# Performance work log

Measured on AMD Instinct MI355X. Metric: run time of the kernel, lower is better.

The kernel has to match this reference:

```python
import jax, jax.numpy as jnp
import numpy as np

B, V_IN, V_OUT, C_IN, C_OUT, K, NNZ = 16, 1024, 4096, 128, 256, 18, 16384

def setup_inputs() -> dict:
    key = jax.random.key(0)
    ks = jax.random.split(key, 10)
    def lin(k, fan_in, fan_out):
        s = 1.0 / np.sqrt(fan_in)
        return jax.random.normal(k, (fan_in, fan_out), jnp.float32) * s
    return {
        "x": jax.random.normal(ks[0], (B, V_IN, C_IN), jnp.float32),
        "vals": jax.random.uniform(ks[1], (NNZ,), jnp.float32),
        "W1": lin(ks[2], 1 * C_IN, C_OUT),
        "b1": jnp.zeros((C_OUT,), jnp.float32),
        "Wd3": lin(ks[3], (K // 3) * C_IN, C_OUT // 4),
        "bd3": jnp.zeros((C_OUT // 4,), jnp.float32),
        "W2d3": lin(ks[4], (K // 3 * 2) * C_IN, C_OUT // 4),
        "b2d3": jnp.zeros((C_OUT // 4,), jnp.float32),
        "Wf": lin(ks[5], K * C_IN, C_OUT // 2),
        "bf": jnp.zeros((C_OUT // 2,), jnp.float32),
        "rows": jax.random.randint(ks[6], (NNZ,), 0, V_OUT, jnp.int32),
        "cols": jax.random.randint(ks[7], (NNZ,), 0, V_IN, jnp.int32),
        "spiral_idx": jax.random.randint(ks[8], (V_OUT, K), 0, V_OUT, jnp.int32),
    }

def _pool(x, rows, cols, vals, dim_size):
    # sparse upsample: gather cols, scale, scatter-add to rows
    gathered = x[:, cols, :] * vals[None, :, None]  # [B, nnz, C]
    return jnp.zeros((x.shape[0], dim_size, x.shape[2]), x.dtype).at[:, rows, :].add(gathered)

def _spiral_conv(feat, idx, W, b):
    # gather fixed spiral neighborhoods then shared linear layer
    Bz, V, C = feat.shape[0], idx.shape[0], feat.shape[2]
    g = feat[:, idx.reshape(-1), :].reshape(Bz, V, idx.shape[1] * C)  # [B, V, K*C]
    return g @ W + b

def reference(x, vals, W1, b1, Wd3, bd3, W2d3, b2d3, Wf, bf, rows, cols, spiral_idx):
    out = _pool(x, rows, cols, vals, V_OUT)  # [B, V_OUT, C_IN]
    k = spiral_idx.shape[1]
    short_cut = _spiral_conv(out, spiral_idx[:, :1], W1, b1)
    p_d3 = _spiral_conv(out, spiral_idx[:, : k // 3], Wd3, bd3)
    p_2d3 = _spiral_conv(out, spiral_idx[:, : k // 3 * 2], W2d3, b2d3)
    p = _spiral_conv(out, spiral_idx, Wf, bf)
    f = jnp.concatenate((p, p_2d3, p_d3), axis=2)  # [B, V_OUT, C_OUT]
    return jax.nn.relu(short_cut + f)
```

## Files before the change

kernel.cpp:

```cpp
#include <hip/hip_runtime.h>
#include <hip/hip_bf16.h>

#define B_SZ   16
#define V_IN   1024
#define V_OUT  4096
#define C_IN   128
#define C_OUT  256
#define K_NB   18
#define NNZ    16384
#define K_GEMM (K_NB * C_IN)
#define BK     64
#define NKT    (K_GEMM / BK)

typedef __attribute__((ext_vector_type(8))) short bf16x8;
typedef __attribute__((ext_vector_type(4))) float f32x4;

#define GLOAD16(src, dst) __builtin_amdgcn_global_load_lds( \
    (const __attribute__((address_space(1))) unsigned int*)(src), \
    (__attribute__((address_space(3))) unsigned int*)(dst), 16, 0, 0)

__global__ void hist_kernel(const int* __restrict__ rows, int* counts) {
    int n = blockIdx.x * blockDim.x + threadIdx.x;
    if (n < NNZ) atomicAdd(&counts[rows[n]], 1);
}

__global__ void scan_kernel(const int* __restrict__ counts, int* offsets, int* cursor) {
    __shared__ int wsum[16];
    int t = threadIdx.x;
    int lane = t & 63, wid = t >> 6;
    int base4 = t * 4;
    int c0 = counts[base4], c1 = counts[base4 + 1], c2 = counts[base4 + 2], c3 = counts[base4 + 3];
    int tot = c0 + c1 + c2 + c3;
    int v = tot;
#pragma unroll
    for (int d = 1; d < 64; d <<= 1) {
        int u = __shfl_up(v, d);
        if (lane >= d) v += u;
    }
    if (lane == 63) wsum[wid] = v;
    __syncthreads();
    int wbase = 0;
#pragma unroll
    for (int w = 0; w < 16; ++w) wbase += (w < wid) ? wsum[w] : 0;
    int incl = wbase + v;
    int excl = incl - tot;
    offsets[base4]     = excl;
    offsets[base4 + 1] = excl + c0;
    offsets[base4 + 2] = excl + c0 + c1;
    offsets[base4 + 3] = excl + c0 + c1 + c2;
    cursor[base4]     = excl;
    cursor[base4 + 1] = excl + c0;
    cursor[base4 + 2] = excl + c0 + c1;
    cursor[base4 + 3] = excl + c0 + c1 + c2;
    if (t == 1023) offsets[V_OUT] = incl;
}

__global__ void fill_kernel(const int* __restrict__ rows, int* cursor, int* perm) {
    int n = blockIdx.x * blockDim.x + threadIdx.x;
    if (n < NNZ) {
        int r = rows[n];
        int pos = atomicAdd(&cursor[r], 1);
        perm[pos] = n;
    }
}

__global__ __launch_bounds__(128) void pool_kernel(
    const float* __restrict__ x, const float* __restrict__ vals,
    const int* __restrict__ cols, const int* __restrict__ offsets,
    const int* __restrict__ perm, __hip_bfloat16* __restrict__ pool) {
    int r = blockIdx.x;
    int c = threadIdx.x;
    int j0 = offsets[r], j1 = offsets[r + 1];
    float acc[B_SZ];
#pragma unroll
    for (int b = 0; b < B_SZ; ++b) acc[b] = 0.f;
    for (int j = j0; j < j1; ++j) {
        int n = perm[j];
        float v = vals[n];
        const float* xp = x + (size_t)cols[n] * C_IN + c;
#pragma unroll
        for (int b = 0; b < B_SZ; ++b) acc[b] += v * xp[(size_t)b * V_IN * C_IN];
    }
#pragma unroll
    for (int b = 0; b < B_SZ; ++b)
        pool[((size_t)b * V_OUT + r) * C_IN + c] = __float2bfloat16(acc[b]);
}

__global__ void wcomb_kernel(const float* __restrict__ W1, const float* __restrict__ Wd3,
                             const float* __restrict__ W2d3, const float* __restrict__ Wf,
                             const float* __restrict__ b1, const float* __restrict__ bd3,
                             const float* __restrict__ b2d3, const float* __restrict__ bf,
                             __hip_bfloat16* __restrict__ wTs, float* __restrict__ bias) {
    int idx = blockIdx.x * blockDim.x + threadIdx.x;
    if (idx >= NKT * 16384) {
        int c = idx - NKT * 16384;
        if (c < C_OUT) {
            float v = b1[c];
            if (c < 128)      v += bf[c];
            else if (c < 192) v += b2d3[c - 128];
            else              v += bd3[c - 192];
            bias[c] = v;
        }
        return;
    }
    int kt = idx >> 14;
    int c  = (idx >> 3) & 2047;
    int e  = idx & 7;
    int nrow  = c >> 3;
    int kslot = (c & 7) << 4;
    int kb = kslot ^ ((nrow & 7) << 4);
    int r  = kt * 64 + (kb >> 1) + e;
    int col = nrow;
    float v;
    if (col < 128)      v = Wf[r * 128 + col];
    else if (col < 192) v = (r < 1536) ? W2d3[r * 64 + (col - 128)] : 0.f;
    else                v = (r < 768)  ? Wd3[r * 64 + (col - 192)]  : 0.f;
    if (r < 128) v += W1[r * 256 + col];
    wTs[idx] = __float2bfloat16(v);
}

__global__ __launch_bounds__(512, 2) void gemm_kernel(
    const __hip_bfloat16* __restrict__ pool,
    const __hip_bfloat16* __restrict__ wTs,
    const float* __restrict__ bias,
    const int* __restrict__ spiral,
    float* __restrict__ out)
{
    __shared__ __align__(16) char smem[149504];
    int* spl = (int*)(smem + 131072);

    const int tid  = threadIdx.x;
    const int lane = tid & 63;
    const int wid  = tid >> 6;
    const int wm   = (wid >> 2) << 7;
    const int wn   = (wid & 3) << 6;
    const int q    = wid & 3;
    const int myNKT = (q == 3) ? 12 : ((q == 2) ? 24 : NKT);

    const int bid = blockIdx.x;
    const int bm  = ((bid & 7) << 5) + (bid >> 3);
    const int b   = bm >> 4;
    const int v0  = (bm & 15) << 8;

    for (int i = tid; i < 256 * K_NB; i += 512) spl[i] = spiral[v0 * K_NB + i];
    asm volatile("s_waitcnt vmcnt(0) lgkmcnt(0)" ::: "memory");
    __builtin_amdgcn_s_barrier();

    const char* poolBytes = (const char*)(pool + (size_t)b * V_OUT * C_IN);
    const char* wTsBytes  = (const char*)wTs;
    const int tg3 = tid >> 3;
    const int sb  = ((tid & 7) << 4) ^ ((tg3 & 7) << 4);

    auto stageA = [&](int kt) {
        const int j   = kt >> 1;
        const int c0b = (kt & 1) << 7;
        char* dst = smem + ((kt & 1) << 15);
#pragma unroll
        for (int ch = 0; ch < 4; ++ch) {
            int sidx = spl[(ch * 64 + tg3) * K_NB + j];
            GLOAD16(poolBytes + ((size_t)sidx << 8) + (c0b + sb),
                    dst + ((ch << 9) + tid) * 16);
        }
    };
    auto stageB = [&](int kt) {
        const char* src = wTsBytes + ((size_t)kt << 15) + tid * 16;
        char* dst = smem + 65536 + ((kt & 1) << 15);
#pragma unroll
        for (int ch = 0; ch < 4; ++ch)
            GLOAD16(src + (ch << 13), dst + (ch << 13) + tid * 16);
    };

    const int l15   = lane & 15;
    const int swm   = (lane & 7) << 4;
    const int klane = (lane >> 4) << 4;
    const int aRow  = (wm + l15) << 7;
    const int bRow  = (wn + l15) << 7;

    f32x4 acc[8][4] = {};

    stageA(0);
    stageB(0);

#pragma unroll 2
    for (int kt = 0; kt < NKT; ++kt) {
        const int s = kt & 1;
        const char* As = smem + (s << 15);
        const char* Bs = smem + 65536 + (s << 15);

        if (kt + 1 < NKT) {
            stageA(kt + 1);
            asm volatile("s_waitcnt vmcnt(4)" ::: "memory");
        } else {
            asm volatile("s_waitcnt vmcnt(0)" ::: "memory");
        }
        __builtin_amdgcn_s_barrier();
        __builtin_amdgcn_sched_barrier(0);

        const bool act = kt < myNKT;
        bf16x8 a[8], b0, b1, b2, b3;

        if (act) {
#pragma unroll
            for (int mi = 0; mi < 8; ++mi)
                a[mi] = *(const bf16x8*)(As + aRow + (mi << 11) + ((0 + klane) ^ swm));
            b0 = *(const bf16x8*)(Bs + bRow + (0 << 11) + ((0 + klane) ^ swm));
            b1 = *(const bf16x8*)(Bs + bRow + (1 << 11) + ((0 + klane) ^ swm));
            __builtin_amdgcn_s_setprio(1);
#pragma unroll
            for (int mi = 0; mi < 8; ++mi) {
                acc[mi][0] = __builtin_amdgcn_mfma_f32_16x16x32_bf16(a[mi], b0, acc[mi][0], 0, 0, 0);
                acc[mi][1] = __builtin_amdgcn_mfma_f32_16x16x32_bf16(a[mi], b1, acc[mi][1], 0, 0, 0);
            }
            __builtin_amdgcn_s_setprio(0);
            b2 = *(const bf16x8*)(Bs + bRow + (2 << 11) + ((0 + klane) ^ swm));
            b3 = *(const bf16x8*)(Bs + bRow + (3 << 11) + ((0 + klane) ^ swm));
            __builtin_amdgcn_s_setprio(1);
#pragma unroll
            for (int mi = 0; mi < 8; ++mi) {
                acc[mi][2] = __builtin_amdgcn_mfma_f32_16x16x32_bf16(a[mi], b2, acc[mi][2], 0, 0, 0);
                acc[mi][3] = __builtin_amdgcn_mfma_f32_16x16x32_bf16(a[mi], b3, acc[mi][3], 0, 0, 0);
            }
            __builtin_amdgcn_s_setprio(0);
        }

        if (kt + 1 < NKT) stageB(kt + 1);

        if (act) {
#pragma unroll
            for (int mi = 0; mi < 8; ++mi)
                a[mi] = *(const bf16x8*)(As + aRow + (mi << 11) + ((64 + klane) ^ swm));
            b0 = *(const bf16x8*)(Bs + bRow + (0 << 11) + ((64 + klane) ^ swm));
            b1 = *(const bf16x8*)(Bs + bRow + (1 << 11) + ((64 + klane) ^ swm));
            __builtin_amdgcn_s_setprio(1);
#pragma unroll
            for (int mi = 0; mi < 8; ++mi) {
                acc[mi][0] = __builtin_amdgcn_mfma_f32_16x16x32_bf16(a[mi], b0, acc[mi][0], 0, 0, 0);
                acc[mi][1] = __builtin_amdgcn_mfma_f32_16x16x32_bf16(a[mi], b1, acc[mi][1], 0, 0, 0);
            }
            __builtin_amdgcn_s_setprio(0);
            b2 = *(const bf16x8*)(Bs + bRow + (2 << 11) + ((64 + klane) ^ swm));
            b3 = *(const bf16x8*)(Bs + bRow + (3 << 11) + ((64 + klane) ^ swm));
            __builtin_amdgcn_s_setprio(1);
#pragma unroll
            for (int mi = 0; mi < 8; ++mi) {
                acc[mi][2] = __builtin_amdgcn_mfma_f32_16x16x32_bf16(a[mi], b2, acc[mi][2], 0, 0, 0);
                acc[mi][3] = __builtin_amdgcn_mfma_f32_16x16x32_bf16(a[mi], b3, acc[mi][3], 0, 0, 0);
            }
            __builtin_amdgcn_s_setprio(0);
        }

        __builtin_amdgcn_s_barrier();
        __builtin_amdgcn_sched_barrier(0);
    }

#pragma unroll
    for (int ni = 0; ni < 4; ++ni) {
        int col = wn + ni * 16 + l15;
        float bz = bias[col];
#pragma unroll
        for (int mi = 0; mi < 8; ++mi) {
            int row0 = v0 + wm + mi * 16 + ((lane >> 4) << 2);
#pragma unroll
            for (int r4 = 0; r4 < 4; ++r4) {
                float v = acc[mi][ni][r4] + bz;
                out[((size_t)(b * V_OUT + row0 + r4)) * C_OUT + col] = v > 0.f ? v : 0.f;
            }
        }
    }
}

extern "C" void kernel_launch(void* const* d_in, const int* in_sizes, int n_in,
                              void* d_out, int out_size, void* d_ws, size_t ws_size,
                              hipStream_t stream) {
    const float* x     = (const float*)d_in[0];
    const float* vals  = (const float*)d_in[1];
    const float* W1    = (const float*)d_in[2];
    const float* b1    = (const float*)d_in[3];
    const float* Wd3   = (const float*)d_in[4];
    const float* bd3   = (const float*)d_in[5];
    const float* W2d3  = (const float*)d_in[6];
    const float* b2d3  = (const float*)d_in[7];
    const float* Wf    = (const float*)d_in[8];
    const float* bf    = (const float*)d_in[9];
    const int*   rows  = (const int*)d_in[10];
    const int*   cols  = (const int*)d_in[11];
    const int*   spiral= (const int*)d_in[12];
    float* out = (float*)d_out;

    char* ws = (char*)d_ws;
    __hip_bfloat16* pool = (__hip_bfloat16*)ws;
    __hip_bfloat16* wTs  = (__hip_bfloat16*)(ws + 16777216);
    float* bias          = (float*)(ws + 16777216 + 1179648);
    int*   counts        = (int*)(ws + 16777216 + 1179648 + 1024);
    int*   offsets       = counts + V_OUT;
    int*   cursor        = offsets + V_OUT + 4;
    int*   perm          = cursor + V_OUT;

    hipMemsetAsync(counts, 0, V_OUT * sizeof(int), stream);
    hist_kernel<<<NNZ / 256, 256, 0, stream>>>(rows, counts);
    scan_kernel<<<1, 1024, 0, stream>>>(counts, offsets, cursor);
    fill_kernel<<<NNZ / 256, 256, 0, stream>>>(rows, cursor, perm);
    pool_kernel<<<V_OUT, C_IN, 0, stream>>>(x, vals, cols, offsets, perm, pool);
    wcomb_kernel<<<(NKT * 16384 + C_OUT + 255) / 256, 256, 0, stream>>>(
        W1, Wd3, W2d3, Wf, b1, bd3, b2d3, bf, wTs, bias);
    gemm_kernel<<<256, 512, 0, stream>>>(pool, wTs, bias, spiral, out);
}
```

Measured before the change: 108.8 us.

## Use 1024-thread GEMM blocks with interleaved column tiles to balance triangular work

The GEMM block grows from 8 to 16 waves. Each wave now owns a 64x64 tile instead of 128x64, and columns are assigned so every wave gets two full-K tiles, one mid-K tile and one short-K tile. Before, whole waves sat idle after 12 or 24 K-steps. The aim is to spread the skipped work evenly across waves and raise MFMA utilisation. The trade-off is half the register reuse per wave, more LDS reads per FLOP, and launch_bounds(1024,4) that may not fit the 149 KB of shared memory.

```diff
diff --git a/kernel.cpp b/kernel.cpp
--- a/kernel.cpp
+++ b/kernel.cpp
@@ -119,7 +119,7 @@
     wTs[idx] = __float2bfloat16(v);
 }
 
-__global__ __launch_bounds__(512, 2) void gemm_kernel(
+__global__ __launch_bounds__(1024, 4) void gemm_kernel(
     const __hip_bfloat16* __restrict__ pool,
     const __hip_bfloat16* __restrict__ wTs,
     const float* __restrict__ bias,
@@ -132,56 +132,57 @@
     const int tid  = threadIdx.x;
     const int lane = tid & 63;
     const int wid  = tid >> 6;
-    const int wm   = (wid >> 2) << 7;
-    const int wn   = (wid & 3) << 6;
-    const int q    = wid & 3;
-    const int myNKT = (q == 3) ? 12 : ((q == 2) ? 24 : NKT);
+    const int wc   = wid & 3;
+    const int wm   = (wid >> 2) << 6;
 
     const int bid = blockIdx.x;
     const int bm  = ((bid & 7) << 5) + (bid >> 3);
     const int b   = bm >> 4;
     const int v0  = (bm & 15) << 8;
 
-    for (int i = tid; i < 256 * K_NB; i += 512) spl[i] = spiral[v0 * K_NB + i];
+    for (int i = tid; i < 256 * K_NB; i += 1024) spl[i] = spiral[v0 * K_NB + i];
     asm volatile("s_waitcnt vmcnt(0) lgkmcnt(0)" ::: "memory");
     __builtin_amdgcn_s_barrier();
 
     const char* poolBytes = (const char*)(pool + (size_t)b * V_OUT * C_IN);
     const char* wTsBytes  = (const char*)wTs;
-    const int tg3 = tid >> 3;
-    const int sb  = ((tid & 7) << 4) ^ ((tg3 & 7) << 4);
+    const int sb = ((tid & 7) << 4) ^ (((tid >> 3) & 7) << 4);
 
     auto stageA = [&](int kt) {
         const int j   = kt >> 1;
         const int c0b = (kt & 1) << 7;
         char* dst = smem + ((kt & 1) << 15);
 #pragma unroll
-        for (int ch = 0; ch < 4; ++ch) {
-            int sidx = spl[(ch * 64 + tg3) * K_NB + j];
-            GLOAD16(poolBytes + ((size_t)sidx << 8) + (c0b + sb),
-                    dst + ((ch << 9) + tid) * 16);
+        for (int ch = 0; ch < 2; ++ch) {
+            int flat = (ch << 10) + tid;
+            int sidx = spl[(flat >> 3) * K_NB + j];
+            GLOAD16(poolBytes + ((size_t)sidx << 8) + (c0b + sb), dst + flat * 16);
         }
     };
     auto stageB = [&](int kt) {
-        const char* src = wTsBytes + ((size_t)kt << 15) + tid * 16;
+        const char* src = wTsBytes + ((size_t)kt << 15);
         char* dst = smem + 65536 + ((kt & 1) << 15);
 #pragma unroll
-        for (int ch = 0; ch < 4; ++ch)
-            GLOAD16(src + (ch << 13), dst + (ch << 13) + tid * 16);
+        for (int ch = 0; ch < 2; ++ch) {
+            int off = ((ch << 10) + tid) << 4;
+            GLOAD16(src + off, dst + off);
+        }
     };
 
     const int l15   = lane & 15;
     const int swm   = (lane & 7) << 4;
     const int klane = (lane >> 4) << 4;
-    const int aRow  = (wm + l15) << 7;
-    const int bRow  = (wn + l15) << 7;
-
-    f32x4 acc[8][4] = {};
+    const int aBase = (wm + l15) << 7;
+    const int bOff0 = (((2 * wc)     << 4) + l15) << 7;
+    const int bOff1 = (((2 * wc + 1) << 4) + l15) << 7;
+    const int bOff2 = (((8 + wc)     << 4) + l15) << 7;
+    const int bOff3 = (((12 + wc)    << 4) + l15) << 7;
+
+    f32x4 acc[4][4] = {};
 
     stageA(0);
     stageB(0);
 
-#pragma unroll 2
     for (int kt = 0; kt < NKT; ++kt) {
         const int s = kt & 1;
         const char* As = smem + (s << 15);
@@ -189,76 +190,67 @@
 
         if (kt + 1 < NKT) {
             stageA(kt + 1);
-            asm volatile("s_waitcnt vmcnt(4)" ::: "memory");
+            asm volatile("s_waitcnt vmcnt(2)" ::: "memory");
         } else {
             asm volatile("s_waitcnt vmcnt(0)" ::: "memory");
         }
         __builtin_amdgcn_s_barrier();
         __builtin_amdgcn_sched_barrier(0);
 
-        const bool act = kt < myNKT;
-        bf16x8 a[8], b0, b1, b2, b3;
-
-        if (act) {
-#pragma unroll
-            for (int mi = 0; mi < 8; ++mi)
-                a[mi] = *(const bf16x8*)(As + aRow + (mi << 11) + ((0 + klane) ^ swm));
-            b0 = *(const bf16x8*)(Bs + bRow + (0 << 11) + ((0 + klane) ^ swm));
-            b1 = *(const bf16x8*)(Bs + bRow + (1 << 11) + ((0 + klane) ^ swm));
+        const bool doMid   = kt < 24;
+        const bool doShort = kt < 12;
+
+#pragma unroll
+        for (int ks = 0; ks < 2; ++ks) {
+            const int kk = (ks * 64 + klane) ^ swm;
+            bf16x8 a0 = *(const bf16x8*)(As + aBase + (0 << 11) + kk);
+            bf16x8 a1 = *(const bf16x8*)(As + aBase + (1 << 11) + kk);
+            bf16x8 a2 = *(const bf16x8*)(As + aBase + (2 << 11) + kk);
+            bf16x8 a3 = *(const bf16x8*)(As + aBase + (3 << 11) + kk);
+            bf16x8 bb0 = *(const bf16x8*)(Bs + bOff0 + kk);
+            bf16x8 bb1 = *(const bf16x8*)(Bs + bOff1 + kk);
             __builtin_amdgcn_s_setprio(1);
-#pragma unroll
-            for (int mi = 0; mi < 8; ++mi) {
-                acc[mi][0] = __builtin_amdgcn_mfma_f32_16x16x32_bf16(a[mi], b0, acc[mi][0], 0, 0, 0);
-                acc[mi][1] = __builtin_amdgcn_mfma_f32_16x16x32_bf16(a[mi], b1, acc[mi][1], 0, 0, 0);
+            acc[0][0] = __builtin_amdgcn_mfma_f32_16x16x32_bf16(a0, bb0, acc[0][0], 0, 0, 0);
+            acc[1][0] = __builtin_amdgcn_mfma_f32_16x16x32_bf16(a1, bb0, acc[1][0], 0, 0, 0);
+            acc[2][0] = __builtin_amdgcn_mfma_f32_16x16x32_bf16(a2, bb0, acc[2][0], 0, 0, 0);
+            acc[3][0] = __builtin_amdgcn_mfma_f32_16x16x32_bf16(a3, bb0, acc[3][0], 0, 0, 0);
+            acc[0][1] = __builtin_amdgcn_mfma_f32_16x16x32_bf16(a0, bb1, acc[0][1], 0, 0, 0);
+            acc[1][1] = __builtin_amdgcn_mfma_f32_16x16x32_bf16(a1, bb1, acc[1][1], 0, 0, 0);
+            acc[2][1] = __builtin_amdgcn_mfma_f32_16x16x32_bf16(a2, bb1, acc[2][1], 0, 0, 0);
+            acc[3][1] = __builtin_amdgcn_mfma_f32_16x16x32_bf16(a3, bb1, acc[3][1], 0, 0, 0);
+            __builtin_amdgcn_s_setprio(0);
+            if (doMid) {
+                bf16x8 bb2 = *(const bf16x8*)(Bs + bOff2 + kk);
+                __builtin_amdgcn_s_setprio(1);
+                acc[0][2] = __builtin_amdgcn_mfma_f32_16x16x32_bf16(a0, bb2, acc[0][2], 0, 0, 0);
+                acc[1][2] = __builtin_amdgcn_mfma_f32_16x16x32_bf16(a1, bb2, acc[1][2], 0, 0, 0);
+                acc[2][2] = __builtin_amdgcn_mfma_f32_16x16x32_bf16(a2, bb2, acc[2][2], 0, 0, 0);
+                acc[3][2] = __builtin_amdgcn_mfma_f32_16x16x32_bf16(a3, bb2, acc[3][2], 0, 0, 0);
+                __builtin_amdgcn_s_setprio(0);
             }
-            __builtin_amdgcn_s_setprio(0);
-            b2 = *(const bf16x8*)(Bs + bRow + (2 << 11) + ((0 + klane) ^ swm));
-            b3 = *(const bf16x8*)(Bs + bRow + (3 << 11) + ((0 + klane) ^ swm));
-            __builtin_amdgcn_s_setprio(1);
-#pragma unroll
-            for (int mi = 0; mi < 8; ++mi) {
-                acc[mi][2] = __builtin_amdgcn_mfma_f32_16x16x32_bf16(a[mi], b2, acc[mi][2], 0, 0, 0);
-                acc[mi][3] = __builtin_amdgcn_mfma_f32_16x16x32_bf16(a[mi], b3, acc[mi][3], 0, 0, 0);
+            if (doShort) {
+                bf16x8 bb3 = *(const bf16x8*)(Bs + bOff3 + kk);
+                __builtin_amdgcn_s_setprio(1);
+                acc[0][3] = __builtin_amdgcn_mfma_f32_16x16x32_bf16(a0, bb3, acc[0][3], 0, 0, 0);
+                acc[1][3] = __builtin_amdgcn_mfma_f32_16x16x32_bf16(a1, bb3, acc[1][3], 0, 0, 0);
+                acc[2][3] = __builtin_amdgcn_mfma_f32_16x16x32_bf16(a2, bb3, acc[2][3], 0, 0, 0);
+                acc[3][3] = __builtin_amdgcn_mfma_f32_16x16x32_bf16(a3, bb3, acc[3][3], 0, 0, 0);
+                __builtin_amdgcn_s_setprio(0);
             }
-            __builtin_amdgcn_s_setprio(0);
-        }
-
-        if (kt + 1 < NKT) stageB(kt + 1);
-
-        if (act) {
-#pragma unroll
-            for (int mi = 0; mi < 8; ++mi)
-                a[mi] = *(const bf16x8*)(As + aRow + (mi << 11) + ((64 + klane) ^ swm));
-            b0 = *(const bf16x8*)(Bs + bRow + (0 << 11) + ((64 + klane) ^ swm));
-            b1 = *(const bf16x8*)(Bs + bRow + (1 << 11) + ((64 + klane) ^ swm));
-            __builtin_amdgcn_s_setprio(1);
-#pragma unroll
-            for (int mi = 0; mi < 8; ++mi) {
-                acc[mi][0] = __builtin_amdgcn_mfma_f32_16x16x32_bf16(a[mi], b0, acc[mi][0], 0, 0, 0);
-                acc[mi][1] = __builtin_amdgcn_mfma_f32_16x16x32_bf16(a[mi], b1, acc[mi][1], 0, 0, 0);
-            }
-            __builtin_amdgcn_s_setprio(0);
-            b2 = *(const bf16x8*)(Bs + bRow + (2 << 11) + ((64 + klane) ^ swm));
-            b3 = *(const bf16x8*)(Bs + bRow + (3 << 11) + ((64 + klane) ^ swm));
-            __builtin_amdgcn_s_setprio(1);
-#pragma unroll
-            for (int mi = 0; mi < 8; ++mi) {
-                acc[mi][2] = __builtin_amdgcn_mfma_f32_16x16x32_bf16(a[mi], b2, acc[mi][2], 0, 0, 0);
-                acc[mi][3] = __builtin_amdgcn_mfma_f32_16x16x32_bf16(a[mi], b3, acc[mi][3], 0, 0, 0);
-            }
-            __builtin_amdgcn_s_setprio(0);
+            if (ks == 0 && kt + 1 < NKT) stageB(kt + 1);
         }
 
         __builtin_amdgcn_s_barrier();
         __builtin_amdgcn_sched_barrier(0);
     }
 
+    const int nt[4] = {2 * wc, 2 * wc + 1, 8 + wc, 12 + wc};
 #pragma unroll
     for (int ni = 0; ni < 4; ++ni) {
-        int col = wn + ni * 16 + l15;
+        int col = (nt[ni] << 4) + l15;
         float bz = bias[col];
 #pragma unroll
-        for (int mi = 0; mi < 8; ++mi) {
+        for (int mi = 0; mi < 4; ++mi) {
             int row0 = v0 + wm + mi * 16 + ((lane >> 4) << 2);
 #pragma unroll
             for (int r4 = 0; r4 < 4; ++r4) {
@@ -303,5 +295,5 @@
     pool_kernel<<<V_OUT, C_IN, 0, stream>>>(x, vals, cols, offsets, perm, pool);
     wcomb_kernel<<<(NKT * 16384 + C_OUT + 255) / 256, 256, 0, stream>>>(
         W1, Wd3, W2d3, Wf, b1, bd3, b2d3, bf, wTs, bias);
-    gemm_kernel<<<256, 512, 0, stream>>>(pool, wTs, bias, spiral, out);
-}
+    gemm_kernel<<<256, 1024, 0, stream>>>(pool, wTs, bias, spiral, out);
+}
```

New measurement: 103.9 us. 4.6% less time.

## Load GEMM B fragments from global, interleave column tiles, triple-buffer A, vectorize pool

Applied to the files above, without the earlier changes.

The GEMM no longer stages weight tiles in LDS. Each wave reads its B fragments straight from global memory (cached in L2), and A moves to a three-slot LDS ring prefetched two steps ahead, which removes the second barrier per iteration. Output column tiles are interleaved across waves so every wave gets equal work on the shortened K ranges of the mid and short branches, replacing the old imbalance where some waves idled. The pool kernel now uses 512 threads with float4 loads, one thread per batch and channel-quad. The risk is higher global-load latency on B fragments that the schedule cannot hide.

```diff
diff --git a/kernel.cpp b/kernel.cpp
--- a/kernel.cpp
+++ b/kernel.cpp
@@ -18,6 +18,8 @@
 #define GLOAD16(src, dst) __builtin_amdgcn_global_load_lds( \
     (const __attribute__((address_space(1))) unsigned int*)(src), \
     (__attribute__((address_space(3))) unsigned int*)(dst), 16, 0, 0)
+
+#define MFMA16(a_, b_, c_) __builtin_amdgcn_mfma_f32_16x16x32_bf16((a_), (b_), (c_), 0, 0, 0)
 
 __global__ void hist_kernel(const int* __restrict__ rows, int* counts) {
     int n = blockIdx.x * blockDim.x + threadIdx.x;
@@ -64,26 +66,28 @@
     }
 }
 
-__global__ __launch_bounds__(128) void pool_kernel(
+__global__ __launch_bounds__(512) void pool_kernel(
     const float* __restrict__ x, const float* __restrict__ vals,
     const int* __restrict__ cols, const int* __restrict__ offsets,
     const int* __restrict__ perm, __hip_bfloat16* __restrict__ pool) {
     int r = blockIdx.x;
-    int c = threadIdx.x;
+    int t = threadIdx.x;
+    int b = t >> 5, c4 = t & 31;
     int j0 = offsets[r], j1 = offsets[r + 1];
-    float acc[B_SZ];
-#pragma unroll
-    for (int b = 0; b < B_SZ; ++b) acc[b] = 0.f;
+    const float4* xb = (const float4*)x + (size_t)b * (V_IN * 32);
+    float4 acc = {0.f, 0.f, 0.f, 0.f};
     for (int j = j0; j < j1; ++j) {
         int n = perm[j];
         float v = vals[n];
-        const float* xp = x + (size_t)cols[n] * C_IN + c;
-#pragma unroll
-        for (int b = 0; b < B_SZ; ++b) acc[b] += v * xp[(size_t)b * V_IN * C_IN];
-    }
-#pragma unroll
-    for (int b = 0; b < B_SZ; ++b)
-        pool[((size_t)b * V_OUT + r) * C_IN + c] = __float2bfloat16(acc[b]);
+        float4 xv = xb[cols[n] * 32 + c4];
+        acc.x += v * xv.x; acc.y += v * xv.y; acc.z += v * xv.z; acc.w += v * xv.w;
+    }
+    ushort4 o;
+    o.x = __builtin_bit_cast(unsigned short, __float2bfloat16(acc.x));
+    o.y = __builtin_bit_cast(unsigned short, __float2bfloat16(acc.y));
+    o.z = __builtin_bit_cast(unsigned short, __float2bfloat16(acc.z));
+    o.w = __builtin_bit_cast(unsigned short, __float2bfloat16(acc.w));
+    ((ushort4*)pool)[((size_t)b * V_OUT + r) * 32 + c4] = o;
 }
 
 __global__ void wcomb_kernel(const float* __restrict__ W1, const float* __restrict__ Wd3,
@@ -126,16 +130,14 @@
     const int* __restrict__ spiral,
     float* __restrict__ out)
 {
-    __shared__ __align__(16) char smem[149504];
-    int* spl = (int*)(smem + 131072);
+    __shared__ __align__(16) char smem[116736];
+    int* spl = (int*)(smem + 98304);
 
     const int tid  = threadIdx.x;
     const int lane = tid & 63;
     const int wid  = tid >> 6;
+    const int q    = wid & 3;
     const int wm   = (wid >> 2) << 7;
-    const int wn   = (wid & 3) << 6;
-    const int q    = wid & 3;
-    const int myNKT = (q == 3) ? 12 : ((q == 2) ? 24 : NKT);
 
     const int bid = blockIdx.x;
     const int bm  = ((bid & 7) << 5) + (bid >> 3);
@@ -148,47 +150,40 @@
 
     const char* poolBytes = (const char*)(pool + (size_t)b * V_OUT * C_IN);
     const char* wTsBytes  = (const char*)wTs;
-    const int tg3 = tid >> 3;
-    const int sb  = ((tid & 7) << 4) ^ ((tg3 & 7) << 4);
-
-    auto stageA = [&](int kt) {
+    const int sb = ((tid & 7) << 4) ^ (((tid >> 3) & 7) << 4);
+
+    auto stageA = [&](int kt, int slot) {
         const int j   = kt >> 1;
         const int c0b = (kt & 1) << 7;
-        char* dst = smem + ((kt & 1) << 15);
+        char* dst = smem + (slot << 15);
 #pragma unroll
         for (int ch = 0; ch < 4; ++ch) {
-            int sidx = spl[(ch * 64 + tg3) * K_NB + j];
+            int row  = (ch << 6) + (tid >> 3);
+            int sidx = spl[row * K_NB + j];
             GLOAD16(poolBytes + ((size_t)sidx << 8) + (c0b + sb),
-                    dst + ((ch << 9) + tid) * 16);
-        }
-    };
-    auto stageB = [&](int kt) {
-        const char* src = wTsBytes + ((size_t)kt << 15) + tid * 16;
-        char* dst = smem + 65536 + ((kt & 1) << 15);
-#pragma unroll
-        for (int ch = 0; ch < 4; ++ch)
-            GLOAD16(src + (ch << 13), dst + (ch << 13) + tid * 16);
+                    dst + (((ch << 9) + tid) << 4));
+        }
     };
 
     const int l15   = lane & 15;
     const int swm   = (lane & 7) << 4;
     const int klane = (lane >> 4) << 4;
-    const int aRow  = (wm + l15) << 7;
-    const int bRow  = (wn + l15) << 7;
+    const int kk0   = klane ^ swm;
+    const int kk1   = (64 + klane) ^ swm;
+    const int aBase = (wm + l15) << 7;
+    const int bOff0 = (((2 * q)     << 4) + l15) << 7;
+    const int bOff1 = (((2 * q + 1) << 4) + l15) << 7;
+    const int bOff2 = (((8 + q)     << 4) + l15) << 7;
+    const int bOff3 = (((12 + q)    << 4) + l15) << 7;
 
     f32x4 acc[8][4] = {};
 
-    stageA(0);
-    stageB(0);
-
-#pragma unroll 2
+    stageA(0, 0);
+    stageA(1, 1);
+
+    int sl = 0;
     for (int kt = 0; kt < NKT; ++kt) {
-        const int s = kt & 1;
-        const char* As = smem + (s << 15);
-        const char* Bs = smem + 65536 + (s << 15);
-
         if (kt + 1 < NKT) {
-            stageA(kt + 1);
             asm volatile("s_waitcnt vmcnt(4)" ::: "memory");
         } else {
             asm volatile("s_waitcnt vmcnt(0)" ::: "memory");
@@ -196,66 +191,74 @@
         __builtin_amdgcn_s_barrier();
         __builtin_amdgcn_sched_barrier(0);
 
-        const bool act = kt < myNKT;
-        bf16x8 a[8], b0, b1, b2, b3;
-
-        if (act) {
-#pragma unroll
-            for (int mi = 0; mi < 8; ++mi)
-                a[mi] = *(const bf16x8*)(As + aRow + (mi << 11) + ((0 + klane) ^ swm));
-            b0 = *(const bf16x8*)(Bs + bRow + (0 << 11) + ((0 + klane) ^ swm));
-            b1 = *(const bf16x8*)(Bs + bRow + (1 << 11) + ((0 + klane) ^ swm));
-            __builtin_amdgcn_s_setprio(1);
-#pragma unroll
-            for (int mi = 0; mi < 8; ++mi) {
-                acc[mi][0] = __builtin_amdgcn_mfma_f32_16x16x32_bf16(a[mi], b0, acc[mi][0], 0, 0, 0);
-                acc[mi][1] = __builtin_amdgcn_mfma_f32_16x16x32_bf16(a[mi], b1, acc[mi][1], 0, 0, 0);
-            }
-            __builtin_amdgcn_s_setprio(0);
-            b2 = *(const bf16x8*)(Bs + bRow + (2 << 11) + ((0 + klane) ^ swm));
-            b3 = *(const bf16x8*)(Bs + bRow + (3 << 11) + ((0 + klane) ^ swm));
-            __builtin_amdgcn_s_setprio(1);
-#pragma unroll
-            for (int mi = 0; mi < 8; ++mi) {
-                acc[mi][2] = __builtin_amdgcn_mfma_f32_16x16x32_bf16(a[mi], b2, acc[mi][2], 0, 0, 0);
-                acc[mi][3] = __builtin_amdgcn_mfma_f32_16x16x32_bf16(a[mi], b3, acc[mi][3], 0, 0, 0);
-            }
-            __builtin_amdgcn_s_setprio(0);
-        }
-
-        if (kt + 1 < NKT) stageB(kt + 1);
-
-        if (act) {
-#pragma unroll
-            for (int mi = 0; mi < 8; ++mi)
-                a[mi] = *(const bf16x8*)(As + aRow + (mi << 11) + ((64 + klane) ^ swm));
-            b0 = *(const bf16x8*)(Bs + bRow + (0 << 11) + ((64 + klane) ^ swm));
-            b1 = *(const bf16x8*)(Bs + bRow + (1 << 11) + ((64 + klane) ^ swm));
-            __builtin_amdgcn_s_setprio(1);
-#pragma unroll
-            for (int mi = 0; mi < 8; ++mi) {
-                acc[mi][0] = __builtin_amdgcn_mfma_f32_16x16x32_bf16(a[mi], b0, acc[mi][0], 0, 0, 0);
-                acc[mi][1] = __builtin_amdgcn_mfma_f32_16x16x32_bf16(a[mi], b1, acc[mi][1], 0, 0, 0);
-            }
-            __builtin_amdgcn_s_setprio(0);
-            b2 = *(const bf16x8*)(Bs + bRow + (2 << 11) + ((64 + klane) ^ swm));
-            b3 = *(const bf16x8*)(Bs + bRow + (3 << 11) + ((64 + klane) ^ swm));
-            __builtin_amdgcn_s_setprio(1);
-#pragma unroll
-            for (int mi = 0; mi < 8; ++mi) {
-                acc[mi][2] = __builtin_amdgcn_mfma_f32_16x16x32_bf16(a[mi], b2, acc[mi][2], 0, 0, 0);
-                acc[mi][3] = __builtin_amdgcn_mfma_f32_16x16x32_bf16(a[mi], b3, acc[mi][3], 0, 0, 0);
-            }
-            __builtin_amdgcn_s_setprio(0);
-        }
-
-        __builtin_amdgcn_s_barrier();
-        __builtin_amdgcn_sched_barrier(0);
-    }
-
+        const char* As  = smem + (sl << 15);
+        const char* wKt = wTsBytes + ((size_t)kt << 15);
+        const bool doMid = kt < 24, doShort = kt < 12;
+
+        bf16x8 b00, b01, b02, b03, b10, b11, b12, b13;
+        b00 = *(const bf16x8*)(wKt + bOff0 + kk0);
+        b01 = *(const bf16x8*)(wKt + bOff1 + kk0);
+        if (doMid)   b02 = *(const bf16x8*)(wKt + bOff2 + kk0);
+        if (doShort) b03 = *(const bf16x8*)(wKt + bOff3 + kk0);
+
+        bf16x8 a[8];
+#pragma unroll
+        for (int mi = 0; mi < 8; ++mi)
+            a[mi] = *(const bf16x8*)(As + aBase + (mi << 11) + kk0);
+
+        b10 = *(const bf16x8*)(wKt + bOff0 + kk1);
+        b11 = *(const bf16x8*)(wKt + bOff1 + kk1);
+        if (doMid)   b12 = *(const bf16x8*)(wKt + bOff2 + kk1);
+        if (doShort) b13 = *(const bf16x8*)(wKt + bOff3 + kk1);
+
+        if (kt + 2 < NKT) {
+            int st = sl + 2; if (st >= 3) st -= 3;
+            stageA(kt + 2, st);
+        }
+
+        __builtin_amdgcn_s_setprio(1);
+#pragma unroll
+        for (int mi = 0; mi < 8; ++mi) {
+            acc[mi][0] = MFMA16(a[mi], b00, acc[mi][0]);
+            acc[mi][1] = MFMA16(a[mi], b01, acc[mi][1]);
+        }
+        if (doMid) {
+#pragma unroll
+            for (int mi = 0; mi < 8; ++mi) acc[mi][2] = MFMA16(a[mi], b02, acc[mi][2]);
+        }
+        if (doShort) {
+#pragma unroll
+            for (int mi = 0; mi < 8; ++mi) acc[mi][3] = MFMA16(a[mi], b03, acc[mi][3]);
+        }
+        __builtin_amdgcn_s_setprio(0);
+
+#pragma unroll
+        for (int mi = 0; mi < 8; ++mi)
+            a[mi] = *(const bf16x8*)(As + aBase + (mi << 11) + kk1);
+
+        __builtin_amdgcn_s_setprio(1);
+#pragma unroll
+        for (int mi = 0; mi < 8; ++mi) {
+            acc[mi][0] = MFMA16(a[mi], b10, acc[mi][0]);
+            acc[mi][1] = MFMA16(a[mi], b11, acc[mi][1]);
+        }
+        if (doMid) {
+#pragma unroll
+            for (int mi = 0; mi < 8; ++mi) acc[mi][2] = MFMA16(a[mi], b12, acc[mi][2]);
+        }
+        if (doShort) {
+#pragma unroll
+            for (int mi = 0; mi < 8; ++mi) acc[mi][3] = MFMA16(a[mi], b13, acc[mi][3]);
+        }
+        __builtin_amdgcn_s_setprio(0);
+
+        sl += 1; if (sl >= 3) sl -= 3;
+    }
+
+    const int nt[4] = {2 * q, 2 * q + 1, 8 + q, 12 + q};
 #pragma unroll
     for (int ni = 0; ni < 4; ++ni) {
-        int col = wn + ni * 16 + l15;
+        int col = (nt[ni] << 4) + l15;
         float bz = bias[col];
 #pragma unroll
         for (int mi = 0; mi < 8; ++mi) {
@@ -300,7 +303,7 @@
     hist_kernel<<<NNZ / 256, 256, 0, stream>>>(rows, counts);
     scan_kernel<<<1, 1024, 0, stream>>>(counts, offsets, cursor);
     fill_kernel<<<NNZ / 256, 256, 0, stream>>>(rows, cursor, perm);
-    pool_kernel<<<V_OUT, C_IN, 0, stream>>>(x, vals, cols, offsets, perm, pool);
+    pool_kernel<<<V_OUT, 512, 0, stream>>>(x, vals, cols, offsets, perm, pool);
     wcomb_kernel<<<(NKT * 16384 + C_OUT + 255) / 256, 256, 0, stream>>>(
         W1, Wd3, W2d3, Wf, b1, bd3, b2d3, bf, wTs, bias);
     gemm_kernel<<<256, 512, 0, stream>>>(pool, wTs, bias, spiral, out);
```

After: 115.0 us. +5.7%, slower.
